# Kernel tuning notes

Measured on AMD Instinct MI355X. Metric: run time of the kernel, lower is better.

Reference implementation:

```python
import jax, jax.numpy as jnp
import numpy as np

VOCAB = 50000
EMB = 128
HID = 256
H = HID // 2          # per-direction LSTM hidden
L = 59                # labelset size
B = 512
S = 256
START, STOP, PAD_LBL = 57, 58, 0
NEG = -10000.0


def setup_inputs() -> dict:
    key = jax.random.key(0)
    ks = jax.random.split(key, 12)
    inp = {}
    inp["x"] = jax.random.randint(ks[0], (B, S), 0, VOCAB)
    inp["y"] = jax.random.randint(ks[1], (B, S), 1, START)  # real labels only
    emb = jax.random.normal(ks[2], (VOCAB, EMB), jnp.float32) * 0.02
    inp["embed"] = emb.at[0].set(0.0)  # padding_idx=0

    def lstm_p(k):
        k1, k2, k3, k4 = jax.random.split(k, 4)
        s = 1.0 / np.sqrt(H)
        return (jax.random.uniform(k1, (4 * H, EMB), jnp.float32, -s, s),
                jax.random.uniform(k2, (4 * H, H), jnp.float32, -s, s),
                jax.random.uniform(k3, (4 * H,), jnp.float32, -s, s),
                jax.random.uniform(k4, (4 * H,), jnp.float32, -s, s))

    inp["Wih_f"], inp["Whh_f"], inp["bih_f"], inp["bhh_f"] = lstm_p(ks[3])
    inp["Wih_b"], inp["Whh_b"], inp["bih_b"], inp["bhh_b"] = lstm_p(ks[4])
    s = 1.0 / np.sqrt(HID)
    inp["Wout"] = jax.random.uniform(ks[5], (L, HID), jnp.float32, -s, s)
    inp["bout"] = jax.random.uniform(ks[6], (L,), jnp.float32, -s, s)
    T = jax.random.normal(ks[7], (L, L), jnp.float32)
    T = T.at[START, :].set(NEG)
    T = T.at[:, STOP].set(NEG)
    T = T.at[START, PAD_LBL].set(NEG)
    T = T.at[STOP + 1:, PAD_LBL].set(NEG)  # no-op here (STOP+1==L), kept for fidelity
    inp["trans"] = T
    inp["h0"] = jax.random.normal(ks[8], (2, B, H), jnp.float32)
    inp["c0"] = jax.random.normal(ks[9], (2, B, H), jnp.float32)
    return inp


def _lstm_scan(emb_seq, Wih, Whh, bih, bhh, h0, c0):
    # emb_seq: (S, B, E); PyTorch gate order i, f, g, o
    def step(carry, x_t):
        h, c = carry
        g = x_t @ Wih.T + bih + h @ Whh.T + bhh          # (B, 4H)
        i, f, gg, o = jnp.split(g, 4, axis=-1)
        c = jax.nn.sigmoid(f) * c + jax.nn.sigmoid(i) * jnp.tanh(gg)
        h = jax.nn.sigmoid(o) * jnp.tanh(c)
        return (h, c), h
    _, hs = jax.lax.scan(step, (h0, c0), emb_seq)
    return hs  # (S, B, H)


def reference(x, y, embed, Wih_f, Whh_f, bih_f, bhh_f,
              Wih_b, Whh_b, bih_b, bhh_b, Wout, bout, trans, h0, c0):
    # ---- BiLSTM emissions ----
    emb = embed[x]                                   # (B, S, E)
    emb = jnp.transpose(emb, (1, 0, 2))              # (S, B, E)
    hf = _lstm_scan(emb, Wih_f, Whh_f, bih_f, bhh_f, h0[0], c0[0])
    hb = _lstm_scan(emb[::-1], Wih_b, Whh_b, bih_b, bhh_b, h0[1], c0[1])[::-1]
    out = jnp.concatenate([hf, hb], axis=-1)         # (S, B, HID)
    feats = jnp.einsum('sbh,lh->bsl', out, Wout) + bout   # (B, S, L)

    # ---- CRF forward algorithm (log-sum-exp scan over time) ----
    alpha0 = jnp.full((B, L), NEG, feats.dtype).at[:, START].set(0.0)
    feats_t = jnp.transpose(feats, (1, 0, 2))        # (S, B, L)

    def fstep(alpha, f_t):
        # alpha_new[b, j] = f_t[b, j] + logsumexp_i(alpha[b, i] + trans[j, i])
        a = jax.nn.logsumexp(alpha[:, None, :] + trans[None, :, :], axis=2)
        return f_t + a, None

    alpha, _ = jax.lax.scan(fstep, alpha0, feats_t)
    fwd_score = jax.nn.logsumexp(alpha + trans[STOP][None, :], axis=1)  # (B,)

    # ---- gold path score ----
    yprev = jnp.concatenate([jnp.full((B, 1), START, y.dtype), y[:, :-1]], axis=1)
    emit = jnp.take_along_axis(feats, y[..., None], axis=2)[..., 0]     # (B, S)
    tr = trans[y, yprev]                                                # (B, S)
    gold = emit.sum(axis=1) + tr.sum(axis=1) + trans[STOP, y[:, -1]]

    return jnp.sum(fwd_score - gold)
```

## Files before the change

kernel.cpp:

```cpp
#include <hip/hip_runtime.h>

#define BB   512
#define SS   256
#define EE   128
#define HH   128
#define LL   59
#define STARTL 57
#define STOPL  58
#define VOCAB 50000

typedef float  f32x4  __attribute__((ext_vector_type(4)));
typedef short  bf16x8 __attribute__((ext_vector_type(8)));
typedef short  s16x4  __attribute__((ext_vector_type(4)));

__device__ __forceinline__ short f2bf(float f) {
    unsigned u = __float_as_uint(f);
    u += 0x7FFFu + ((u >> 16) & 1u);
    return (short)(u >> 16);
}
__device__ __forceinline__ float bf2f(unsigned short s) {
    return __uint_as_float(((unsigned)s) << 16);
}
__device__ __forceinline__ float sigf(float x) {
    float e = __builtin_amdgcn_exp2f(-1.44269504f * x);
    return __builtin_amdgcn_rcpf(1.0f + e);
}
__device__ __forceinline__ float tanhf_(float x) {
    float e = __builtin_amdgcn_exp2f(2.88539008f * x);
    return 1.0f - 2.0f * __builtin_amdgcn_rcpf(e + 1.0f);
}
__device__ __forceinline__ float wmax64(float v) {
    #pragma unroll
    for (int o = 32; o; o >>= 1) v = fmaxf(v, __shfl_xor(v, o));
    return v;
}
__device__ __forceinline__ float wsum64(float v) {
    #pragma unroll
    for (int o = 32; o; o >>= 1) v += __shfl_xor(v, o);
    return v;
}
__device__ __forceinline__ void bar_lds() {
    asm volatile("s_waitcnt lgkmcnt(0)\n\ts_barrier" ::: "memory");
}

__global__ __launch_bounds__(256) void conv_k(
    const float* __restrict__ embed,
    const float* __restrict__ Wih_f, const float* __restrict__ Wih_b,
    const float* __restrict__ Whh_f, const float* __restrict__ Whh_b,
    const float* __restrict__ bih_f, const float* __restrict__ bhh_f,
    const float* __restrict__ bih_b, const float* __restrict__ bhh_b,
    unsigned short* __restrict__ ebf, unsigned short* __restrict__ wix,
    unsigned short* __restrict__ whb, float* __restrict__ bsum)
{
    const int W1 = VOCAB * EE / 4;
    const int W2 = W1 + 2 * 16384;
    const int W3 = W2 + 2 * 16384;
    const int W4 = W3 + 1024;
    for (int i = blockIdx.x * blockDim.x + threadIdx.x; i < W4;
         i += gridDim.x * blockDim.x) {
        if (i < W1) {
            float4 v = ((const float4*)embed)[i];
            s16x4 s = { f2bf(v.x), f2bf(v.y), f2bf(v.z), f2bf(v.w) };
            ((s16x4*)ebf)[i] = s;
        } else if (i < W2) {
            const int j = i - W1, d = j >> 14, e = j & 16383;
            float4 v = ((const float4*)(d ? Wih_b : Wih_f))[e];
            s16x4 s = { f2bf(v.x), f2bf(v.y), f2bf(v.z), f2bf(v.w) };
            ((s16x4*)wix)[d * 16384 + e] = s;
        } else if (i < W3) {
            const int j = i - W2, d = j >> 14, e = j & 16383;
            float4 v = ((const float4*)(d ? Whh_b : Whh_f))[e];
            s16x4 s = { f2bf(v.x), f2bf(v.y), f2bf(v.z), f2bf(v.w) };
            ((s16x4*)whb)[d * 16384 + e] = s;
        } else {
            const int m = i - W3, d = m >> 9, c = m & 511;
            bsum[d * 512 + c] = d ? (bih_b[c] + bhh_b[c]) : (bih_f[c] + bhh_f[c]);
        }
    }
}

__global__ __launch_bounds__(512, 2) void lstm_f(
    const int* __restrict__ x, const unsigned short* __restrict__ ebf,
    const unsigned short* __restrict__ wix, const unsigned short* __restrict__ whb,
    const float* __restrict__ bsum,
    const float* __restrict__ h0, const float* __restrict__ c0,
    const float* __restrict__ Wout,
    unsigned short* __restrict__ fpF, unsigned short* __restrict__ fpB)
{
    const int tid = threadIdx.x;
    const int w = tid >> 6, l = tid & 63, qd = l >> 4, n = l & 15;
    const int rt = blockIdx.x & 127, dir = blockIdx.x >> 7;
    const int b0 = rt * 4;
    unsigned short* fp = dir ? fpB : fpF;

    __shared__ __align__(16) short hbuf[2][2048];
    __shared__ __align__(16) float gxb[2][4][2048];
    __shared__ int xsh[4 * 256];

    #pragma unroll
    for (int i = 0; i < 2; ++i) ((s16x4*)hbuf)[tid + i * 512] = (s16x4)0;
    #pragma unroll
    for (int i = 0; i < 2; ++i) {
        const int k = tid + i * 512;
        xsh[k] = x[(size_t)(b0 + (k >> 8)) * SS + (k & 255)];
    }

    if (w < 4) {
        const int s0 = 2 * w, s1 = 2 * w + 1;
        bf16x8 fh0[4][4], fh1[4][4];
        #pragma unroll
        for (int g = 0; g < 4; ++g) {
            #pragma unroll
            for (int kk = 0; kk < 4; ++kk) {
                fh0[g][kk] = *(const bf16x8*)(whb + dir * 65536
                             + (size_t)(g * 128 + 16 * s0 + n) * 128 + kk * 32 + qd * 8);
                fh1[g][kk] = *(const bf16x8*)(whb + dir * 65536
                             + (size_t)(g * 128 + 16 * s1 + n) * 128 + kk * 32 + qd * 8);
            }
        }
        bf16x8 wb[4];
        {
            const int col = w * 16 + n;
            #pragma unroll
            for (int kk = 0; kk < 4; ++kk) {
                bf16x8 v = (bf16x8)0;
                if (col < LL) {
                    const float* p = Wout + (size_t)col * 256 + dir * 128 + kk * 32 + qd * 8;
                    #pragma unroll
                    for (int j = 0; j < 8; ++j) v[j] = f2bf(p[j]);
                }
                wb[kk] = v;
            }
        }
        float cst0 = c0[((size_t)dir * BB + b0 + qd) * HH + 16 * s0 + n];
        float cst1 = c0[((size_t)dir * BB + b0 + qd) * HH + 16 * s1 + n];

        __syncthreads();
        {
            const int j = tid >> 7, c = tid & 127;
            hbuf[0][((c >> 3) * 16 + 4 * j) * 8 + (c & 7)] =
                f2bf(h0[((size_t)dir * BB + b0 + j) * HH + c]);
        }
        __syncthreads();

        const int hid0 = 16 * s0 + n, hc0 = hid0 >> 3, ho0 = hid0 & 7;
        const int hid1 = 16 * s1 + n, hc1 = hid1 >> 3, ho1 = hid1 & 7;
        const int gs0 = (s0 * 64 + qd * 16 + n) * 4;
        const int gs1 = (s1 * 64 + qd * 16 + n) * 4;

        f32x4 a0[4], a1[4], pa;
        #pragma unroll
        for (int g = 0; g < 4; ++g) {
            a0[g] = (f32x4){0.f, 0.f, 0.f, 0.f};
            a1[g] = (f32x4){0.f, 0.f, 0.f, 0.f};
        }
        pa = (f32x4){0.f, 0.f, 0.f, 0.f};

        unsigned short* fpp = fp + ((size_t)(b0 + qd) * SS + (dir ? SS - 1 : 0)) * 64
                            + w * 16 + n;
        const ptrdiff_t fpd = dir ? -64 : 64;

        for (int ts = 0; ts < SS; ++ts) {
            const int cur = ts & 1, nxt = cur ^ 1;
            const int gbuf = (ts >> 2) & 1, tau = ts & 3;

            const f32x4 g0 = *(const f32x4*)&gxb[gbuf][tau][gs0];
            const f32x4 g1 = *(const f32x4*)&gxb[gbuf][tau][gs1];

            bf16x8 ah[4];
            #pragma unroll
            for (int kk = 0; kk < 4; ++kk)
                ah[kk] = *(const bf16x8*)&hbuf[cur][((kk * 4 + qd) * 16 + n) * 8];

            a0[0][0] = g0[0]; a0[1][0] = g0[1]; a0[2][0] = g0[2]; a0[3][0] = g0[3];
            a1[0][0] = g1[0]; a1[1][0] = g1[1]; a1[2][0] = g1[2]; a1[3][0] = g1[3];

            #pragma unroll
            for (int kk = 0; kk < 4; ++kk) {
                #pragma unroll
                for (int g = 0; g < 4; ++g) {
                    a0[g] = __builtin_amdgcn_mfma_f32_16x16x32_bf16(ah[kk], fh0[g][kk], a0[g], 0, 0, 0);
                    a1[g] = __builtin_amdgcn_mfma_f32_16x16x32_bf16(ah[kk], fh1[g][kk], a1[g], 0, 0, 0);
                }
            }

            if (ts > 0) {
                pa[0] = 0.f;
                #pragma unroll
                for (int kk = 0; kk < 4; ++kk)
                    pa = __builtin_amdgcn_mfma_f32_16x16x32_bf16(ah[kk], wb[kk], pa, 0, 0, 0);
                *fpp = (unsigned short)f2bf(pa[0]);
                fpp += fpd;
            }

            {
                const float iv0 = sigf(a0[0][0]), fv0 = sigf(a0[1][0]);
                const float gv0 = tanhf_(a0[2][0]), ov0 = sigf(a0[3][0]);
                const float cc0 = fv0 * cst0 + iv0 * gv0;
                cst0 = cc0;
                hbuf[nxt][(hc0 * 16 + 4 * qd) * 8 + ho0] = f2bf(ov0 * tanhf_(cc0));
                const float iv1 = sigf(a1[0][0]), fv1 = sigf(a1[1][0]);
                const float gv1 = tanhf_(a1[2][0]), ov1 = sigf(a1[3][0]);
                const float cc1 = fv1 * cst1 + iv1 * gv1;
                cst1 = cc1;
                hbuf[nxt][(hc1 * 16 + 4 * qd) * 8 + ho1] = f2bf(ov1 * tanhf_(cc1));
            }
            bar_lds();
        }

        {
            pa[0] = 0.f;
            #pragma unroll
            for (int kk = 0; kk < 4; ++kk) {
                const bf16x8 a = *(const bf16x8*)&hbuf[0][((kk * 4 + qd) * 16 + n) * 8];
                pa = __builtin_amdgcn_mfma_f32_16x16x32_bf16(a, wb[kk], pa, 0, 0, 0);
            }
            *fpp = (unsigned short)f2bf(pa[0]);
        }
    } else {
        const int s0 = 2 * (w - 4), s1 = s0 + 1;
        bf16x8 fx0[4][4], fx1[4][4]; float bs0[4], bs1[4];
        #pragma unroll
        for (int g = 0; g < 4; ++g) {
            bs0[g] = bsum[dir * 512 + g * 128 + 16 * s0 + n];
            bs1[g] = bsum[dir * 512 + g * 128 + 16 * s1 + n];
            #pragma unroll
            for (int kk = 0; kk < 4; ++kk) {
                fx0[g][kk] = *(const bf16x8*)(wix + dir * 65536
                             + (size_t)(g * 128 + 16 * s0 + n) * 128 + kk * 32 + qd * 8);
                fx1[g][kk] = *(const bf16x8*)(wix + dir * 65536
                             + (size_t)(g * 128 + 16 * s1 + n) * 128 + kk * 32 + qd * 8);
            }
        }
        const int gs0 = (s0 * 64 + qd * 16 + n) * 4;
        const int gs1 = (s1 * 64 + qd * 16 + n) * 4;
        const int jb   = n >> 2;
        const int tau  = n & 3;
        const int jrow = jb * 256;

        auto loadfrag = [&](int G, bf16x8* e) {
            const int t  = 4 * G + tau;
            const int te = dir ? (SS - 1 - t) : t;
            const int xi = xsh[jrow + te];
            const unsigned short* er = ebf + (size_t)xi * EE + qd * 8;
            e[0] = *(const bf16x8*)(er);
            e[1] = *(const bf16x8*)(er + 32);
            e[2] = *(const bf16x8*)(er + 64);
            e[3] = *(const bf16x8*)(er + 96);
        };
        auto computeS = [&](const bf16x8* e, const bf16x8 (*fx)[4],
                            const float* bs, int gsv, int buf) {
            f32x4 c[4] = { {0,0,0,0}, {0,0,0,0}, {0,0,0,0}, {0,0,0,0} };
            #pragma unroll
            for (int g = 0; g < 4; ++g) {
                #pragma unroll
                for (int kk = 0; kk < 4; ++kk)
                    c[g] = __builtin_amdgcn_mfma_f32_16x16x32_bf16(e[kk], fx[g][kk], c[g], 0, 0, 0);
            }
            #pragma unroll
            for (int r = 0; r < 4; ++r) {
                f32x4 p = { c[0][r] + bs[0], c[1][r] + bs[1],
                            c[2][r] + bs[2], c[3][r] + bs[3] };
                *(f32x4*)&gxb[buf][r][gsv] = p;
            }
        };

        __syncthreads();
        bf16x8 eA[4], eB[4];
        loadfrag(0, eA);
        computeS(eA, fx0, bs0, gs0, 0);
        computeS(eA, fx1, bs1, gs1, 0);
        loadfrag(1, eB);
        __syncthreads();

        auto xgroup = [&](int G, bf16x8* use, bf16x8* pre) {
            if (G + 2 < SS / 4) loadfrag(G + 2, pre);
            if (G + 1 < SS / 4) computeS(use, fx0, bs0, gs0, (G + 1) & 1);
            bar_lds();
            if (G + 1 < SS / 4) computeS(use, fx1, bs1, gs1, (G + 1) & 1);
            bar_lds();
            bar_lds();
            bar_lds();
        };
        for (int G = 0; G < SS / 4; G += 2) {
            xgroup(G,     eB, eA);
            xgroup(G + 1, eA, eB);
        }
    }
}

__global__ __launch_bounds__(64, 1) void crf_k(
    const unsigned short* __restrict__ fpF, const unsigned short* __restrict__ fpB,
    const float* __restrict__ bout, const int* __restrict__ y,
    const float* __restrict__ trans, float* __restrict__ out)
{
    const int j = threadIdx.x;
    const int b = blockIdx.x;
    const size_t bS = (size_t)b * SS;
    const bool valid = (j < LL);
    const int  jr = valid ? j : (LL - 1);

    float etr[LL];
    #pragma unroll
    for (int i = 0; i < LL; ++i) {
        const float t = trans[jr * LL + i];
        etr[i] = valid ? __builtin_amdgcn_exp2f(t * 1.44269504f) : 0.0f;
    }
    const float bo = valid ? bout[jr] : 0.0f;

    float alpha = valid ? ((j == STARTL) ? 0.0f : -10000.0f) : -1e30f;

    float fF[8], fB[8];
    #pragma unroll
    for (int q = 0; q < 8; ++q) {
        fF[q] = bf2f(fpF[(bS + q) * 64 + j]);
        fB[q] = bf2f(fpB[(bS + q) * 64 + j]);
    }

    for (int t0 = 0; t0 < SS; t0 += 8) {
        float nF[8], nB[8];
        #pragma unroll
        for (int q = 0; q < 8; ++q) { nF[q] = 0.0f; nB[q] = 0.0f; }
        if (t0 + 8 < SS) {
            #pragma unroll
            for (int q = 0; q < 8; ++q) {
                nF[q] = bf2f(fpF[(bS + t0 + 8 + q) * 64 + j]);
                nB[q] = bf2f(fpB[(bS + t0 + 8 + q) * 64 + j]);
            }
        }
        #pragma unroll
        for (int u = 0; u < 8; ++u) {
            const float K = fmaxf(
                __uint_as_float(__builtin_amdgcn_readlane(__float_as_uint(alpha), 1)),
                __uint_as_float(__builtin_amdgcn_readlane(__float_as_uint(alpha), STARTL)));
            const float ea = __builtin_amdgcn_exp2f((alpha - K) * 1.44269504f);
            float d0 = 0.0f, d1 = 0.0f, d2 = 0.0f, d3 = 0.0f;
            #pragma unroll
            for (int i = 0; i < LL; i += 4) {
                d0 += etr[i] * __uint_as_float(__builtin_amdgcn_readlane(__float_as_uint(ea), i));
                if (i + 1 < LL) d1 += etr[i+1] * __uint_as_float(__builtin_amdgcn_readlane(__float_as_uint(ea), i+1));
                if (i + 2 < LL) d2 += etr[i+2] * __uint_as_float(__builtin_amdgcn_readlane(__float_as_uint(ea), i+2));
                if (i + 3 < LL) d3 += etr[i+3] * __uint_as_float(__builtin_amdgcn_readlane(__float_as_uint(ea), i+3));
            }
            const float dot = (d0 + d1) + (d2 + d3);
            alpha = (fF[u] + fB[u] + bo) + K + 0.69314718f * __builtin_amdgcn_logf(dot);
        }
        #pragma unroll
        for (int q = 0; q < 8; ++q) { fF[q] = nF[q]; fB[q] = nB[q]; }
    }

    const float v  = alpha + trans[STOPL * LL + jr];
    const float m2 = wmax64(v);
    const float s  = wsum64(__builtin_amdgcn_exp2f((v - m2) * 1.44269504f));
    const float fwd = m2 + 0.69314718f * __builtin_amdgcn_logf(s);

    float g = 0.0f;
    #pragma unroll
    for (int q = 0; q < 4; ++q) {
        const int t  = q * 64 + j;
        const int yt = y[bS + t];
        const int yp = t ? y[bS + t - 1] : STARTL;
        g += bf2f(fpF[(bS + t) * 64 + yt]) + bf2f(fpB[(bS + t) * 64 + yt])
           + bout[yt] + trans[yt * LL + yp];
    }
    g = wsum64(g);

    if (j == 0) {
        g += trans[STOPL * LL + y[bS + SS - 1]];
        atomicAdd(out, fwd - g);
    }
}

extern "C" void kernel_launch(void* const* d_in, const int* in_sizes, int n_in,
                              void* d_out, int out_size, void* d_ws, size_t ws_size,
                              hipStream_t stream)
{
    (void)in_sizes; (void)n_in; (void)out_size; (void)ws_size;
    const int*   x      = (const int*)  d_in[0];
    const int*   y      = (const int*)  d_in[1];
    const float* embed  = (const float*)d_in[2];
    const float* Wih_f  = (const float*)d_in[3];
    const float* Whh_f  = (const float*)d_in[4];
    const float* bih_f  = (const float*)d_in[5];
    const float* bhh_f  = (const float*)d_in[6];
    const float* Wih_b  = (const float*)d_in[7];
    const float* Whh_b  = (const float*)d_in[8];
    const float* bih_b  = (const float*)d_in[9];
    const float* bhh_b  = (const float*)d_in[10];
    const float* Wout   = (const float*)d_in[11];
    const float* bout   = (const float*)d_in[12];
    const float* trans  = (const float*)d_in[13];
    const float* h0     = (const float*)d_in[14];
    const float* c0     = (const float*)d_in[15];

    const size_t MiB = 1ull << 20;
    unsigned short* fpF  = (unsigned short*)d_ws;
    unsigned short* fpB  = (unsigned short*)((char*)d_ws + 16 * MiB);
    unsigned short* ebf  = (unsigned short*)((char*)d_ws + 32 * MiB);
    unsigned short* wix  = (unsigned short*)((char*)d_ws + 45 * MiB);
    unsigned short* whb  = (unsigned short*)((char*)d_ws + 45 * MiB + 256 * 1024);
    float*          bsum = (float*)((char*)d_ws + 45 * MiB + 512 * 1024);

    hipMemsetAsync(d_out, 0, sizeof(float), stream);
    conv_k<<<2048, 256, 0, stream>>>(embed, Wih_f, Wih_b, Whh_f, Whh_b,
                                     bih_f, bhh_f, bih_b, bhh_b,
                                     ebf, wix, whb, bsum);
    lstm_f<<<256, 512, 0, stream>>>(x, ebf, wix, whb, bsum, h0, c0, Wout,
                                    fpF, fpB);
    crf_k<<<BB, 64, 0, stream>>>(fpF, fpB, bout, y, trans, (float*)d_out);
}
```

Baseline: 393.7 us.

## Double LSTM block to 1024 threads with one hidden slot per wave

The LSTM kernel now launches 1024 threads per block, and each of 16 waves owns a single 16-column hidden slot instead of two. Recurrent waves and input-projection waves are interleaved by wave index. The Wout projection fragments are moved from registers into shared memory, and the x-projection loop is restructured to split its MFMA work across barrier phases. The aim is to shorten the serial per-timestep critical path by spreading the recurrent MFMAs across more waves. The cost is extra per-step barrier participants and LDS reads for the output weights.

```diff
diff --git a/kernel.cpp b/kernel.cpp
--- a/kernel.cpp
+++ b/kernel.cpp
@@ -79,7 +79,7 @@
     }
 }
 
-__global__ __launch_bounds__(512, 2) void lstm_f(
+__global__ __launch_bounds__(1024, 4) void lstm_f(
     const int* __restrict__ x, const unsigned short* __restrict__ ebf,
     const unsigned short* __restrict__ wix, const unsigned short* __restrict__ whb,
     const float* __restrict__ bsum,
@@ -93,153 +93,119 @@
     const int b0 = rt * 4;
     unsigned short* fp = dir ? fpB : fpF;
 
+    const int role = (w ^ (w >> 2)) & 1;
+    const int slot = ((w & 8) >> 1) | ((w & 7) >> 1);
+
     __shared__ __align__(16) short hbuf[2][2048];
     __shared__ __align__(16) float gxb[2][4][2048];
+    __shared__ __align__(16) short wbl[4][4][512];
     __shared__ int xsh[4 * 256];
 
-    #pragma unroll
-    for (int i = 0; i < 2; ++i) ((s16x4*)hbuf)[tid + i * 512] = (s16x4)0;
-    #pragma unroll
-    for (int i = 0; i < 2; ++i) {
-        const int k = tid + i * 512;
-        xsh[k] = x[(size_t)(b0 + (k >> 8)) * SS + (k & 255)];
-    }
-
-    if (w < 4) {
-        const int s0 = 2 * w, s1 = 2 * w + 1;
-        bf16x8 fh0[4][4], fh1[4][4];
-        #pragma unroll
-        for (int g = 0; g < 4; ++g) {
-            #pragma unroll
-            for (int kk = 0; kk < 4; ++kk) {
-                fh0[g][kk] = *(const bf16x8*)(whb + dir * 65536
-                             + (size_t)(g * 128 + 16 * s0 + n) * 128 + kk * 32 + qd * 8);
-                fh1[g][kk] = *(const bf16x8*)(whb + dir * 65536
-                             + (size_t)(g * 128 + 16 * s1 + n) * 128 + kk * 32 + qd * 8);
-            }
-        }
-        bf16x8 wb[4];
-        {
-            const int col = w * 16 + n;
-            #pragma unroll
-            for (int kk = 0; kk < 4; ++kk) {
-                bf16x8 v = (bf16x8)0;
-                if (col < LL) {
-                    const float* p = Wout + (size_t)col * 256 + dir * 128 + kk * 32 + qd * 8;
-                    #pragma unroll
-                    for (int j = 0; j < 8; ++j) v[j] = f2bf(p[j]);
-                }
-                wb[kk] = v;
-            }
-        }
-        float cst0 = c0[((size_t)dir * BB + b0 + qd) * HH + 16 * s0 + n];
-        float cst1 = c0[((size_t)dir * BB + b0 + qd) * HH + 16 * s1 + n];
-
-        __syncthreads();
-        {
+    ((s16x4*)hbuf)[tid] = (s16x4)0;
+    xsh[tid] = x[(size_t)(b0 + (tid >> 8)) * SS + (tid & 255)];
+    {
+        const int pt = tid >> 8, kkw = (tid >> 6) & 3, ln = tid & 63;
+        const int col = pt * 16 + (ln & 15), qw = ln >> 4;
+        s16x4 lo = (s16x4)0, hi = (s16x4)0;
+        if (col < LL) {
+            const float* p = Wout + (size_t)col * 256 + dir * 128 + kkw * 32 + qw * 8;
+            lo = (s16x4){ f2bf(p[0]), f2bf(p[1]), f2bf(p[2]), f2bf(p[3]) };
+            hi = (s16x4){ f2bf(p[4]), f2bf(p[5]), f2bf(p[6]), f2bf(p[7]) };
+        }
+        *(s16x4*)&wbl[pt][kkw][ln * 8]     = lo;
+        *(s16x4*)&wbl[pt][kkw][ln * 8 + 4] = hi;
+    }
+    __syncthreads();
+
+    if (role == 0) {
+        bf16x8 fh[4][4];
+        #pragma unroll
+        for (int g = 0; g < 4; ++g)
+            #pragma unroll
+            for (int kk = 0; kk < 4; ++kk)
+                fh[g][kk] = *(const bf16x8*)(whb + dir * 65536
+                            + (size_t)(g * 128 + 16 * slot + n) * 128 + kk * 32 + qd * 8);
+        float cst = c0[((size_t)dir * BB + b0 + qd) * HH + 16 * slot + n];
+
+        if (tid < 512) {
             const int j = tid >> 7, c = tid & 127;
             hbuf[0][((c >> 3) * 16 + 4 * j) * 8 + (c & 7)] =
                 f2bf(h0[((size_t)dir * BB + b0 + j) * HH + c]);
         }
         __syncthreads();
 
-        const int hid0 = 16 * s0 + n, hc0 = hid0 >> 3, ho0 = hid0 & 7;
-        const int hid1 = 16 * s1 + n, hc1 = hid1 >> 3, ho1 = hid1 & 7;
-        const int gs0 = (s0 * 64 + qd * 16 + n) * 4;
-        const int gs1 = (s1 * 64 + qd * 16 + n) * 4;
-
-        f32x4 a0[4], a1[4], pa;
-        #pragma unroll
-        for (int g = 0; g < 4; ++g) {
-            a0[g] = (f32x4){0.f, 0.f, 0.f, 0.f};
-            a1[g] = (f32x4){0.f, 0.f, 0.f, 0.f};
-        }
+        const int hid = 16 * slot + n, hc = hid >> 3, ho = hid & 7;
+        const int gs = (slot * 64 + qd * 16 + n) * 4;
+        const bool doproj = (slot < 4);
+
+        f32x4 a[4], pa;
+        #pragma unroll
+        for (int g = 0; g < 4; ++g) a[g] = (f32x4){0.f, 0.f, 0.f, 0.f};
         pa = (f32x4){0.f, 0.f, 0.f, 0.f};
 
         unsigned short* fpp = fp + ((size_t)(b0 + qd) * SS + (dir ? SS - 1 : 0)) * 64
-                            + w * 16 + n;
+                            + slot * 16 + n;
         const ptrdiff_t fpd = dir ? -64 : 64;
 
         for (int ts = 0; ts < SS; ++ts) {
             const int cur = ts & 1, nxt = cur ^ 1;
             const int gbuf = (ts >> 2) & 1, tau = ts & 3;
 
-            const f32x4 g0 = *(const f32x4*)&gxb[gbuf][tau][gs0];
-            const f32x4 g1 = *(const f32x4*)&gxb[gbuf][tau][gs1];
-
-            bf16x8 ah[4];
+            const f32x4 g0 = *(const f32x4*)&gxb[gbuf][tau][gs];
+            a[0][0] = g0[0]; a[1][0] = g0[1]; a[2][0] = g0[2]; a[3][0] = g0[3];
+            const bool pj = doproj && (ts > 0);
+            if (pj) pa[0] = 0.f;
+
+            #pragma unroll
+            for (int kk = 0; kk < 4; ++kk) {
+                const bf16x8 ah = *(const bf16x8*)&hbuf[cur][((kk * 4 + qd) * 16 + n) * 8];
+                a[0] = __builtin_amdgcn_mfma_f32_16x16x32_bf16(ah, fh[0][kk], a[0], 0, 0, 0);
+                a[1] = __builtin_amdgcn_mfma_f32_16x16x32_bf16(ah, fh[1][kk], a[1], 0, 0, 0);
+                a[2] = __builtin_amdgcn_mfma_f32_16x16x32_bf16(ah, fh[2][kk], a[2], 0, 0, 0);
+                a[3] = __builtin_amdgcn_mfma_f32_16x16x32_bf16(ah, fh[3][kk], a[3], 0, 0, 0);
+                if (pj) {
+                    const bf16x8 wb = *(const bf16x8*)&wbl[slot][kk][l * 8];
+                    pa = __builtin_amdgcn_mfma_f32_16x16x32_bf16(ah, wb, pa, 0, 0, 0);
+                }
+            }
+            if (pj) { *fpp = (unsigned short)f2bf(pa[0]); fpp += fpd; }
+
+            {
+                const float iv = sigf(a[0][0]), fv = sigf(a[1][0]);
+                const float gv = tanhf_(a[2][0]), ov = sigf(a[3][0]);
+                const float cc = fv * cst + iv * gv;
+                cst = cc;
+                hbuf[nxt][(hc * 16 + 4 * qd) * 8 + ho] = f2bf(ov * tanhf_(cc));
+            }
+            bar_lds();
+        }
+
+        if (doproj) {
+            pa[0] = 0.f;
+            #pragma unroll
+            for (int kk = 0; kk < 4; ++kk) {
+                const bf16x8 ah = *(const bf16x8*)&hbuf[0][((kk * 4 + qd) * 16 + n) * 8];
+                const bf16x8 wb = *(const bf16x8*)&wbl[slot][kk][l * 8];
+                pa = __builtin_amdgcn_mfma_f32_16x16x32_bf16(ah, wb, pa, 0, 0, 0);
+            }
+            *fpp = (unsigned short)f2bf(pa[0]);
+        }
+    } else {
+        bf16x8 fx[4][4]; float bs[4];
+        #pragma unroll
+        for (int g = 0; g < 4; ++g) {
+            bs[g] = bsum[dir * 512 + g * 128 + 16 * slot + n];
             #pragma unroll
             for (int kk = 0; kk < 4; ++kk)
-                ah[kk] = *(const bf16x8*)&hbuf[cur][((kk * 4 + qd) * 16 + n) * 8];
-
-            a0[0][0] = g0[0]; a0[1][0] = g0[1]; a0[2][0] = g0[2]; a0[3][0] = g0[3];
-            a1[0][0] = g1[0]; a1[1][0] = g1[1]; a1[2][0] = g1[2]; a1[3][0] = g1[3];
-
-            #pragma unroll
-            for (int kk = 0; kk < 4; ++kk) {
-                #pragma unroll
-                for (int g = 0; g < 4; ++g) {
-                    a0[g] = __builtin_amdgcn_mfma_f32_16x16x32_bf16(ah[kk], fh0[g][kk], a0[g], 0, 0, 0);
-                    a1[g] = __builtin_amdgcn_mfma_f32_16x16x32_bf16(ah[kk], fh1[g][kk], a1[g], 0, 0, 0);
-                }
-            }
-
-            if (ts > 0) {
-                pa[0] = 0.f;
-                #pragma unroll
-                for (int kk = 0; kk < 4; ++kk)
-                    pa = __builtin_amdgcn_mfma_f32_16x16x32_bf16(ah[kk], wb[kk], pa, 0, 0, 0);
-                *fpp = (unsigned short)f2bf(pa[0]);
-                fpp += fpd;
-            }
-
-            {
-                const float iv0 = sigf(a0[0][0]), fv0 = sigf(a0[1][0]);
-                const float gv0 = tanhf_(a0[2][0]), ov0 = sigf(a0[3][0]);
-                const float cc0 = fv0 * cst0 + iv0 * gv0;
-                cst0 = cc0;
-                hbuf[nxt][(hc0 * 16 + 4 * qd) * 8 + ho0] = f2bf(ov0 * tanhf_(cc0));
-                const float iv1 = sigf(a1[0][0]), fv1 = sigf(a1[1][0]);
-                const float gv1 = tanhf_(a1[2][0]), ov1 = sigf(a1[3][0]);
-                const float cc1 = fv1 * cst1 + iv1 * gv1;
-                cst1 = cc1;
-                hbuf[nxt][(hc1 * 16 + 4 * qd) * 8 + ho1] = f2bf(ov1 * tanhf_(cc1));
-            }
-            bar_lds();
-        }
-
-        {
-            pa[0] = 0.f;
-            #pragma unroll
-            for (int kk = 0; kk < 4; ++kk) {
-                const bf16x8 a = *(const bf16x8*)&hbuf[0][((kk * 4 + qd) * 16 + n) * 8];
-                pa = __builtin_amdgcn_mfma_f32_16x16x32_bf16(a, wb[kk], pa, 0, 0, 0);
-            }
-            *fpp = (unsigned short)f2bf(pa[0]);
-        }
-    } else {
-        const int s0 = 2 * (w - 4), s1 = s0 + 1;
-        bf16x8 fx0[4][4], fx1[4][4]; float bs0[4], bs1[4];
-        #pragma unroll
-        for (int g = 0; g < 4; ++g) {
-            bs0[g] = bsum[dir * 512 + g * 128 + 16 * s0 + n];
-            bs1[g] = bsum[dir * 512 + g * 128 + 16 * s1 + n];
-            #pragma unroll
-            for (int kk = 0; kk < 4; ++kk) {
-                fx0[g][kk] = *(const bf16x8*)(wix + dir * 65536
-                             + (size_t)(g * 128 + 16 * s0 + n) * 128 + kk * 32 + qd * 8);
-                fx1[g][kk] = *(const bf16x8*)(wix + dir * 65536
-                             + (size_t)(g * 128 + 16 * s1 + n) * 128 + kk * 32 + qd * 8);
-            }
-        }
-        const int gs0 = (s0 * 64 + qd * 16 + n) * 4;
-        const int gs1 = (s1 * 64 + qd * 16 + n) * 4;
-        const int jb   = n >> 2;
-        const int tau  = n & 3;
+                fx[g][kk] = *(const bf16x8*)(wix + dir * 65536
+                            + (size_t)(g * 128 + 16 * slot + n) * 128 + kk * 32 + qd * 8);
+        }
+        const int gs = (slot * 64 + qd * 16 + n) * 4;
+        const int jb = n >> 2, taur = n & 3;
         const int jrow = jb * 256;
 
         auto loadfrag = [&](int G, bf16x8* e) {
-            const int t  = 4 * G + tau;
+            const int t  = 4 * G + taur;
             const int te = dir ? (SS - 1 - t) : t;
             const int xi = xsh[jrow + te];
             const unsigned short* er = ebf + (size_t)xi * EE + qd * 8;
@@ -248,43 +214,57 @@
             e[2] = *(const bf16x8*)(er + 64);
             e[3] = *(const bf16x8*)(er + 96);
         };
-        auto computeS = [&](const bf16x8* e, const bf16x8 (*fx)[4],
-                            const float* bs, int gsv, int buf) {
+
+        bf16x8 eA[4];
+        loadfrag(0, eA);
+        {
             f32x4 c[4] = { {0,0,0,0}, {0,0,0,0}, {0,0,0,0}, {0,0,0,0} };
             #pragma unroll
-            for (int g = 0; g < 4; ++g) {
+            for (int g = 0; g < 4; ++g)
                 #pragma unroll
                 for (int kk = 0; kk < 4; ++kk)
-                    c[g] = __builtin_amdgcn_mfma_f32_16x16x32_bf16(e[kk], fx[g][kk], c[g], 0, 0, 0);
-            }
+                    c[g] = __builtin_amdgcn_mfma_f32_16x16x32_bf16(eA[kk], fx[g][kk], c[g], 0, 0, 0);
             #pragma unroll
             for (int r = 0; r < 4; ++r) {
                 f32x4 p = { c[0][r] + bs[0], c[1][r] + bs[1],
                             c[2][r] + bs[2], c[3][r] + bs[3] };
-                *(f32x4*)&gxb[buf][r][gsv] = p;
-            }
-        };
-
+                *(f32x4*)&gxb[0][r][gs] = p;
+            }
+        }
+        loadfrag(1, eA);
         __syncthreads();
-        bf16x8 eA[4], eB[4];
-        loadfrag(0, eA);
-        computeS(eA, fx0, bs0, gs0, 0);
-        computeS(eA, fx1, bs1, gs1, 0);
-        loadfrag(1, eB);
-        __syncthreads();
-
-        auto xgroup = [&](int G, bf16x8* use, bf16x8* pre) {
-            if (G + 2 < SS / 4) loadfrag(G + 2, pre);
-            if (G + 1 < SS / 4) computeS(use, fx0, bs0, gs0, (G + 1) & 1);
-            bar_lds();
-            if (G + 1 < SS / 4) computeS(use, fx1, bs1, gs1, (G + 1) & 1);
-            bar_lds();
-            bar_lds();
-            bar_lds();
-        };
-        for (int G = 0; G < SS / 4; G += 2) {
-            xgroup(G,     eB, eA);
-            xgroup(G + 1, eA, eB);
+
+        f32x4 c[4];
+        for (int G = 0; G < SS / 4; ++G) {
+            const int nb = (G + 1) & 1;
+            const bool produce = (G + 1 < SS / 4);
+            if (produce) {
+                #pragma unroll
+                for (int g = 0; g < 4; ++g) c[g] = (f32x4){0.f, 0.f, 0.f, 0.f};
+                #pragma unroll
+                for (int kk = 0; kk < 2; ++kk)
+                    #pragma unroll
+                    for (int g = 0; g < 4; ++g)
+                        c[g] = __builtin_amdgcn_mfma_f32_16x16x32_bf16(eA[kk], fx[g][kk], c[g], 0, 0, 0);
+            }
+            bar_lds();
+            if (produce) {
+                #pragma unroll
+                for (int kk = 2; kk < 4; ++kk)
+                    #pragma unroll
+                    for (int g = 0; g < 4; ++g)
+                        c[g] = __builtin_amdgcn_mfma_f32_16x16x32_bf16(eA[kk], fx[g][kk], c[g], 0, 0, 0);
+                #pragma unroll
+                for (int r = 0; r < 4; ++r) {
+                    f32x4 p = { c[0][r] + bs[0], c[1][r] + bs[1],
+                                c[2][r] + bs[2], c[3][r] + bs[3] };
+                    *(f32x4*)&gxb[nb][r][gs] = p;
+                }
+            }
+            bar_lds();
+            if (G + 2 < SS / 4) loadfrag(G + 2, eA);
+            bar_lds();
+            bar_lds();
         }
     }
 }
@@ -405,7 +385,7 @@
     conv_k<<<2048, 256, 0, stream>>>(embed, Wih_f, Wih_b, Whh_f, Whh_b,
                                      bih_f, bhh_f, bih_b, bhh_b,
                                      ebf, wix, whb, bsum);
-    lstm_f<<<256, 512, 0, stream>>>(x, ebf, wix, whb, bsum, h0, c0, Wout,
-                                    fpF, fpB);
+    lstm_f<<<256, 1024, 0, stream>>>(x, ebf, wix, whb, bsum, h0, c0, Wout,
+                                     fpF, fpB);
     crf_k<<<BB, 64, 0, stream>>>(fpF, fpB, bout, y, trans, (float*)d_out);
 }
```

After: 400.1 us. No clear change (+1.6%).
